# Kernel optimization log

Measured on AMD Instinct MI355X. Metric: run time of the kernel, lower is better.

## Reference

```python
import jax, jax.numpy as jnp
import numpy as np

B, C, H, W = 2, 64, 270, 480
CQ = C // 8


def _distance_weight(n):
    i = jnp.arange(n, dtype=jnp.float32)
    d = i[None, :] - i[:, None]  # j - i
    return jnp.exp(-(d * d) / (2.0 * (n * n / 4.0)))  # [n, n]


def setup_inputs() -> dict:
    key = jax.random.key(0)
    ks = jax.random.split(key, 8)
    s = 0.05
    return {
        "x": jax.random.normal(ks[0], (B, C, H, W), jnp.float32),
        "Wq": jax.random.normal(ks[1], (CQ, C), jnp.float32) * s,
        "bq": jax.random.normal(ks[2], (CQ,), jnp.float32) * s,
        "Wk": jax.random.normal(ks[3], (CQ, C), jnp.float32) * s,
        "bk": jax.random.normal(ks[4], (CQ,), jnp.float32) * s,
        "Wv": jax.random.normal(ks[5], (C, C), jnp.float32) * s,
        "bv": jax.random.normal(ks[6], (C,), jnp.float32) * s,
        "gamma": jax.random.normal(ks[7], (), jnp.float32) * 0.3,
        "dw_h": _distance_weight(H),  # [H, H] non-trainable buffer
        "dw_w": _distance_weight(W),  # [W, W] non-trainable buffer
    }


def reference(x, Wq, bq, Wk, bk, Wv, bv, gamma, dw_h, dw_w):
    # 1x1 convs == per-pixel linear projections
    q = jnp.einsum('oc,bchw->bohw', Wq, x) + bq[None, :, None, None]  # [B,CQ,H,W]
    k = jnp.einsum('oc,bchw->bohw', Wk, x) + bk[None, :, None, None]  # [B,CQ,H,W]
    v = jnp.einsum('oc,bchw->bohw', Wv, x) + bv[None, :, None, None]  # [B,C,H,W]

    height, width = x.shape[2], x.shape[3]
    neg_inf = jnp.float32(-jnp.inf)

    # row (H-direction) energy: queries/keys along the height axis per column w
    e_h = jnp.einsum('bchw,bcgw->bwhg', q, k) * dw_h[None, None]  # [B,W,H,H]
    # diagonal -inf mask (dw_h diag == 1, so order of mul is immaterial)
    eye_h = jnp.eye(height, dtype=bool)
    e_h = jnp.where(eye_h[None, None], neg_inf, e_h)
    e_h = jnp.transpose(e_h, (0, 2, 1, 3))  # [B,H,W,H]

    # column (W-direction) energy along the width axis per row h
    e_w = jnp.einsum('bchw,bchv->bhwv', q, k) * dw_w[None, None]  # [B,H,W,W]

    # joint softmax over concatenated H and W directions
    att = jax.nn.softmax(jnp.concatenate([e_h, e_w], axis=3), axis=3)  # [B,H,W,H+W]
    att_h = jnp.transpose(att[:, :, :, :height], (0, 2, 1, 3))  # [B,W,H,H]
    att_w = att[:, :, :, height:]  # [B,H,W,W]

    out_h = jnp.einsum('bcgw,bwhg->bchw', v, att_h)  # [B,C,H,W]
    out_w = jnp.einsum('bchv,bhwv->bchw', v, att_w)  # [B,C,H,W]

    return gamma * (out_h + out_w) + x
```

## Files before the change

kernel.cpp:

```cpp
#include <hip/hip_runtime.h>
#include <hip/hip_bf16.h>

namespace {

constexpr int B  = 2;
constexpr int C  = 64;
constexpr int CQ = 8;
constexpr int H  = 270;
constexpr int W  = 480;
constexpr int HW = H * W;
constexpr float INVH2 = 2.0f / (270.0f * 270.0f);
constexpr float INVW2 = 2.0f / (480.0f * 480.0f);

typedef __attribute__((ext_vector_type(4))) float f32x4;
typedef __attribute__((ext_vector_type(8))) short short8;
typedef __attribute__((ext_vector_type(4))) unsigned int uint4v;

__device__ __forceinline__ float bits2f(unsigned short u) {
  union { unsigned int i; float f; } cv;
  cv.i = ((unsigned int)u) << 16;
  return cv.f;
}

__device__ __forceinline__ unsigned short f2bf(float f) {
  union { __hip_bfloat16 b; unsigned short u; } cv;
  cv.b = __float2bfloat16(f);
  return cv.u;
}

__device__ __forceinline__ unsigned int pack2(float a, float b) {
  return ((unsigned int)f2bf(b) << 16) | (unsigned int)f2bf(a);
}

__device__ __forceinline__ short8 pack_p(const float p0[4], const float p1[4]) {
  uint4v pw;
  pw[0] = pack2(p0[0], p0[1]);
  pw[1] = pack2(p0[2], p0[3]);
  pw[2] = pack2(p1[0], p1[1]);
  pw[3] = pack2(p1[2], p1[3]);
  return __builtin_bit_cast(short8, pw);
}


__global__ __launch_bounds__(256)
void k_qkv(const float* __restrict__ x,
           const float* __restrict__ Wq, const float* __restrict__ bq,
           const float* __restrict__ Wk, const float* __restrict__ bk,
           const float* __restrict__ Wv, const float* __restrict__ bv,
           unsigned short* __restrict__ qwp, unsigned short* __restrict__ kwp,
           unsigned short* __restrict__ qhp, unsigned short* __restrict__ khp,
           unsigned short* __restrict__ v, unsigned short* __restrict__ vt) {
  __shared__ __align__(16) float wql[CQ * C];
  __shared__ __align__(16) float wkl[CQ * C];
  __shared__ __align__(16) float wvl[C * C];
  __shared__ float bql[CQ], bkl[CQ], bvl[C];
  const int tid = threadIdx.x;
  for (int i = tid; i < CQ * C; i += 256) { wql[i] = Wq[i]; wkl[i] = Wk[i]; }
  for (int i = tid; i < C * C; i += 256) wvl[i] = Wv[i];
  if (tid < CQ) { bql[tid] = bq[tid]; bkl[tid] = bk[tid]; }
  if (tid < C) bvl[tid] = bv[tid];
  __syncthreads();
  const int pix = blockIdx.x * 256 + tid;
  if (pix >= B * HW) return;
  const int b = pix / HW;
  const int r = pix - b * HW;
  const int h = r / W;
  const int w = r - h * W;

  float qa[CQ], ka[CQ], va[C];
#pragma unroll
  for (int o = 0; o < CQ; ++o) { qa[o] = bql[o]; ka[o] = bkl[o]; }
#pragma unroll
  for (int o = 0; o < C; ++o) va[o] = bvl[o];

  const float* xp = x + (size_t)b * C * HW + r;
  for (int c = 0; c < C; c += 4) {
    const float x0 = xp[(size_t)(c + 0) * HW];
    const float x1 = xp[(size_t)(c + 1) * HW];
    const float x2 = xp[(size_t)(c + 2) * HW];
    const float x3 = xp[(size_t)(c + 3) * HW];
#pragma unroll
    for (int o = 0; o < CQ; ++o) {
      const float4 a = *(const float4*)(wql + o * C + c);
      qa[o] = fmaf(a.w, x3, fmaf(a.z, x2, fmaf(a.y, x1, fmaf(a.x, x0, qa[o]))));
      const float4 bb = *(const float4*)(wkl + o * C + c);
      ka[o] = fmaf(bb.w, x3, fmaf(bb.z, x2, fmaf(bb.y, x1, fmaf(bb.x, x0, ka[o]))));
    }
#pragma unroll
    for (int o = 0; o < C; ++o) {
      const float4 cc = *(const float4*)(wvl + o * C + c);
      va[o] = fmaf(cc.w, x3, fmaf(cc.z, x2, fmaf(cc.y, x1, fmaf(cc.x, x0, va[o]))));
    }
  }

  uint4 qp4, kp4;
  qp4.x = pack2(qa[0], qa[1]); qp4.y = pack2(qa[2], qa[3]);
  qp4.z = pack2(qa[4], qa[5]); qp4.w = pack2(qa[6], qa[7]);
  kp4.x = pack2(ka[0], ka[1]); kp4.y = pack2(ka[2], ka[3]);
  kp4.z = pack2(ka[4], ka[5]); kp4.w = pack2(ka[6], ka[7]);
  *(uint4*)(qwp + (size_t)pix * 8) = qp4;
  *(uint4*)(kwp + (size_t)pix * 8) = kp4;
  const size_t tbase = ((size_t)b * W + w) * H + h;
  *(uint4*)(qhp + tbase * 8) = qp4;
  *(uint4*)(khp + tbase * 8) = kp4;

  unsigned short* vp = v + (size_t)b * C * HW + r;
#pragma unroll
  for (int o = 0; o < C; ++o) vp[(size_t)o * HW] = f2bf(va[o]);
  unsigned short* vtp = vt + tbase * C;
#pragma unroll
  for (int j = 0; j < 16; ++j) {
    ushort4 u;
    u.x = f2bf(va[4 * j + 0]);
    u.y = f2bf(va[4 * j + 1]);
    u.z = f2bf(va[4 * j + 2]);
    u.w = f2bf(va[4 * j + 3]);
    *(ushort4*)(vtp + 4 * j) = u;
  }
}

constexpr int VSW = 494;

__global__ __launch_bounds__(512, 1)
void k_outw(const unsigned short* __restrict__ qwp,
            const unsigned short* __restrict__ kwp,
            const unsigned short* __restrict__ v,
            unsigned short* __restrict__ ow, float* __restrict__ Sw) {
  __shared__ __align__(16) unsigned short vbs[64 * VSW];
  __shared__ __align__(16) unsigned short kls[480 * 8];
  const int h = blockIdx.x >> 1, z = blockIdx.x & 1;
  const int b = blockIdx.y;
  const int tid = threadIdx.x;
  const size_t rowbase = ((size_t)b * H + h) * W;

  const unsigned short* vrow = v + (size_t)b * C * HW + (size_t)h * W;
  for (int idx = tid; idx < 64 * 120; idx += 512) {
    const int c = idx / 120, s4 = (idx - c * 120) * 4;
    const int u = s4 & 31;
    const int t = (u < 16) ? ((u >> 2) * 8) : (((u - 16) >> 2) * 8 + 4);
    *(ushort4*)(vbs + c * VSW + (s4 & ~31) + t) =
        *(const ushort4*)(vrow + (size_t)c * HW + s4);
  }
  for (int g = tid; g < 480; g += 512)
    *(uint4*)(kls + g * 8) = *(const uint4*)(kwp + (rowbase + g) * 8);

  const int lane = tid & 63, wv = tid >> 6;
  const int l15 = lane & 15, quad = lane >> 4;
  const int chunk = z * 8 + wv;
  const bool active = chunk < 15;
  const int m0 = chunk * 32;

  short8 qa0 = short8{0, 0, 0, 0, 0, 0, 0, 0};
  short8 qa1 = short8{0, 0, 0, 0, 0, 0, 0, 0};
  if (quad == 0 && active) {
    qa0 = *(const short8*)(qwp + (rowbase + m0 + l15) * 8);
    qa1 = *(const short8*)(qwp + (rowbase + m0 + 16 + l15) * 8);
  }

  f32x4 acc[2][4];
  float Sacc[2] = {0.0f, 0.0f};
#pragma unroll
  for (int mt = 0; mt < 2; ++mt)
#pragma unroll
    for (int ct = 0; ct < 4; ++ct)
#pragma unroll
      for (int rr = 0; rr < 4; ++rr) acc[mt][ct][rr] = 0.0f;

  __syncthreads();

  if (active) {
    for (int ci = 0; ci < 15; ++ci) {
      const int sc = ci * 32;
      short8 kb0 = short8{0, 0, 0, 0, 0, 0, 0, 0};
      short8 kb1 = short8{0, 0, 0, 0, 0, 0, 0, 0};
      if (quad == 0) {
        kb0 = *(const short8*)(kls + (sc + l15) * 8);
        kb1 = *(const short8*)(kls + (sc + 16 + l15) * 8);
      }
      const f32x4 z4 = f32x4{0.f, 0.f, 0.f, 0.f};
      const f32x4 E00 = __builtin_amdgcn_mfma_f32_16x16x32_bf16(kb0, qa0, z4, 0, 0, 0);
      const f32x4 E01 = __builtin_amdgcn_mfma_f32_16x16x32_bf16(kb1, qa0, z4, 0, 0, 0);
      const f32x4 E10 = __builtin_amdgcn_mfma_f32_16x16x32_bf16(kb0, qa1, z4, 0, 0, 0);
      const f32x4 E11 = __builtin_amdgcn_mfma_f32_16x16x32_bf16(kb1, qa1, z4, 0, 0, 0);
      short8 vb[4];
#pragma unroll
      for (int ct = 0; ct < 4; ++ct)
        vb[ct] = *(const short8*)(vbs + (ct * 16 + l15) * VSW + sc + quad * 8);
#pragma unroll
      for (int mt = 0; mt < 2; ++mt) {
        const int m = m0 + mt * 16 + l15;
        const f32x4 Ea = mt ? E10 : E00;
        const f32x4 Eb = mt ? E11 : E01;
        float p0[4], p1[4];
#pragma unroll
        for (int rr = 0; rr < 4; ++rr) {
          const float d0 = (float)(m - (sc + quad * 4 + rr));
          const float d1 = d0 - 16.0f;
          p0[rr] = __expf(Ea[rr] * __expf(-(d0 * d0) * INVW2));
          p1[rr] = __expf(Eb[rr] * __expf(-(d1 * d1) * INVW2));
          Sacc[mt] += p0[rr] + p1[rr];
        }
        const short8 pa = pack_p(p0, p1);
#pragma unroll
        for (int ct = 0; ct < 4; ++ct)
          acc[mt][ct] = __builtin_amdgcn_mfma_f32_16x16x32_bf16(pa, vb[ct], acc[mt][ct], 0, 0, 0);
      }
    }

#pragma unroll
    for (int mt = 0; mt < 2; ++mt) {
      float s = Sacc[mt];
      s += __shfl_xor(s, 16);
      s += __shfl_xor(s, 32);
      if (lane < 16) Sw[rowbase + m0 + mt * 16 + l15] = s;
    }
  }

  __syncthreads();
  unsigned short* ob = vbs;
  if (active) {
#pragma unroll
    for (int mt = 0; mt < 2; ++mt)
#pragma unroll
      for (int ct = 0; ct < 4; ++ct)
#pragma unroll
        for (int rr = 0; rr < 4; ++rr)
          ob[(ct * 16 + l15) * VSW + m0 + mt * 16 + quad * 4 + rr] = f2bf(acc[mt][ct][rr]);
  }
  __syncthreads();
  unsigned short* og = ow + ((size_t)b * H + h) * C * W;
  const int mlo = z ? 256 : 0;
  const int nu = z ? 112 : 128;
  for (int idx = tid; idx < 64 * nu; idx += 512) {
    const int c = idx / nu, i = idx - c * nu;
    *(unsigned int*)(og + (size_t)c * W + mlo + 2 * i) =
        *(const unsigned int*)(ob + c * VSW + mlo + 2 * i);
  }
}

constexpr int VSH = 302;

__global__ __launch_bounds__(320, 1)
void k_outh(const unsigned short* __restrict__ qhp,
            const unsigned short* __restrict__ khp,
            const unsigned short* __restrict__ vt,
            unsigned short* __restrict__ oht, float* __restrict__ Sht) {
  __shared__ __align__(16) unsigned short vbs[64 * VSH];
  __shared__ __align__(16) unsigned short kls[288 * 8];
  const int w = blockIdx.x >> 1, z = blockIdx.x & 1;
  const int b = blockIdx.y;
  const int tid = threadIdx.x;
  const size_t colbase = ((size_t)b * W + w) * H;

  const unsigned short* vtb = vt + colbase * C;
  for (int idx = tid; idx < 288 * 16; idx += 320) {
    const int g = idx >> 4, c4 = (idx & 15) * 4;
    ushort4 vv = make_ushort4(0, 0, 0, 0);
    if (g < H) vv = *(const ushort4*)(vtb + (size_t)g * C + c4);
    const int u = g & 31;
    const int t = (u < 16) ? ((u >> 2) * 8 + (u & 3))
                           : (((u - 16) >> 2) * 8 + 4 + (u & 3));
    const int slot = (g & ~31) + t;
    vbs[(c4 + 0) * VSH + slot] = vv.x;
    vbs[(c4 + 1) * VSH + slot] = vv.y;
    vbs[(c4 + 2) * VSH + slot] = vv.z;
    vbs[(c4 + 3) * VSH + slot] = vv.w;
  }
  for (int g = tid; g < 288; g += 320)
    *(uint4*)(kls + g * 8) =
        *(const uint4*)(khp + (colbase + min(g, H - 1)) * 8);

  const int lane = tid & 63, wv = tid >> 6;
  const int l15 = lane & 15, quad = lane >> 4;
  const int chunk = z * 5 + wv;
  const bool active = chunk < 9;
  const int m0 = chunk * 32;

  short8 qa0 = short8{0, 0, 0, 0, 0, 0, 0, 0};
  short8 qa1 = short8{0, 0, 0, 0, 0, 0, 0, 0};
  if (quad == 0 && active) {
    qa0 = *(const short8*)(qhp + (colbase + min(m0 + l15, H - 1)) * 8);
    qa1 = *(const short8*)(qhp + (colbase + min(m0 + 16 + l15, H - 1)) * 8);
  }

  f32x4 acc[2][4];
  float Sacc[2] = {0.0f, 0.0f};
#pragma unroll
  for (int mt = 0; mt < 2; ++mt)
#pragma unroll
    for (int ct = 0; ct < 4; ++ct)
#pragma unroll
      for (int rr = 0; rr < 4; ++rr) acc[mt][ct][rr] = 0.0f;

  __syncthreads();

  if (active) {
    for (int ci = 0; ci < 9; ++ci) {
      const int gc = ci * 32;
      short8 kb0 = short8{0, 0, 0, 0, 0, 0, 0, 0};
      short8 kb1 = short8{0, 0, 0, 0, 0, 0, 0, 0};
      if (quad == 0) {
        kb0 = *(const short8*)(kls + (gc + l15) * 8);
        kb1 = *(const short8*)(kls + (gc + 16 + l15) * 8);
      }
      const f32x4 z4 = f32x4{0.f, 0.f, 0.f, 0.f};
      const f32x4 E00 = __builtin_amdgcn_mfma_f32_16x16x32_bf16(kb0, qa0, z4, 0, 0, 0);
      const f32x4 E01 = __builtin_amdgcn_mfma_f32_16x16x32_bf16(kb1, qa0, z4, 0, 0, 0);
      const f32x4 E10 = __builtin_amdgcn_mfma_f32_16x16x32_bf16(kb0, qa1, z4, 0, 0, 0);
      const f32x4 E11 = __builtin_amdgcn_mfma_f32_16x16x32_bf16(kb1, qa1, z4, 0, 0, 0);
      short8 vb[4];
#pragma unroll
      for (int ct = 0; ct < 4; ++ct)
        vb[ct] = *(const short8*)(vbs + (ct * 16 + l15) * VSH + gc + quad * 8);
#pragma unroll
      for (int mt = 0; mt < 2; ++mt) {
        const int m = m0 + mt * 16 + l15;
        const f32x4 Ea = mt ? E10 : E00;
        const f32x4 Eb = mt ? E11 : E01;
        float p0[4], p1[4];
#pragma unroll
        for (int rr = 0; rr < 4; ++rr) {
          const int g0 = gc + quad * 4 + rr;
          const int g1 = g0 + 16;
          const float d0 = (float)(m - g0);
          const float d1 = d0 - 16.0f;
          p0[rr] = (g0 < H && g0 != m)
                       ? __expf(Ea[rr] * __expf(-(d0 * d0) * INVH2)) : 0.0f;
          p1[rr] = (g1 < H && g1 != m)
                       ? __expf(Eb[rr] * __expf(-(d1 * d1) * INVH2)) : 0.0f;
          Sacc[mt] += p0[rr] + p1[rr];
        }
        const short8 pa = pack_p(p0, p1);
#pragma unroll
        for (int ct = 0; ct < 4; ++ct)
          acc[mt][ct] = __builtin_amdgcn_mfma_f32_16x16x32_bf16(pa, vb[ct], acc[mt][ct], 0, 0, 0);
      }
    }

#pragma unroll
    for (int mt = 0; mt < 2; ++mt) {
      float s = Sacc[mt];
      s += __shfl_xor(s, 16);
      s += __shfl_xor(s, 32);
      const int m = m0 + mt * 16 + l15;
      if (lane < 16 && m < H) Sht[colbase + m] = s;
    }
  }

  __syncthreads();
  unsigned short* ob = vbs;
  if (active) {
#pragma unroll
    for (int mt = 0; mt < 2; ++mt)
#pragma unroll
      for (int ct = 0; ct < 4; ++ct)
#pragma unroll
        for (int rr = 0; rr < 4; ++rr)
          ob[(ct * 16 + l15) * VSH + m0 + mt * 16 + quad * 4 + rr] = f2bf(acc[mt][ct][rr]);
  }
  __syncthreads();
  unsigned short* og = oht + ((size_t)b * W + w) * C * H;
  const int mlo = z ? 160 : 0;
  const int nu = z ? 55 : 80;
  for (int idx = tid; idx < 64 * nu; idx += 320) {
    const int c = idx / nu, i = idx - c * nu;
    *(unsigned int*)(og + (size_t)c * H + mlo + 2 * i) =
        *(const unsigned int*)(ob + c * VSH + mlo + 2 * i);
  }
}

__global__ __launch_bounds__(256)
void k_combine(const unsigned short* __restrict__ oht,
               const unsigned short* __restrict__ ow,
               const float* __restrict__ Sht, const float* __restrict__ Sw,
               const float* __restrict__ x,
               const float* __restrict__ gp,
               float* __restrict__ out) {
  __shared__ float tile[32][33];
  const int b = blockIdx.z >> 6, c = blockIdx.z & 63;
  const int w0 = blockIdx.x * 32, h0 = blockIdx.y * 32;
  const int tx = threadIdx.x, ty = threadIdx.y;
#pragma unroll
  for (int i = 0; i < 4; ++i) {
    const int wl = ty + i * 8;
    const int hh = h0 + tx;
    float val = 0.0f;
    if (hh < H) val = bits2f(oht[(((size_t)b * W + (w0 + wl)) * C + c) * H + hh]);
    tile[wl][tx] = val;
  }
  __syncthreads();
  const float gamma = *gp;
#pragma unroll
  for (int i = 0; i < 4; ++i) {
    const int hl = ty + i * 8;
    const int hh = h0 + hl;
    if (hh < H) {
      const int ww = w0 + tx;
      const float uh = tile[tx][hl];
      const float uw = bits2f(ow[(((size_t)b * H + hh) * C + c) * W + ww]);
      const size_t si = ((size_t)b * H + hh) * W + ww;
      const float Z = Sht[((size_t)b * W + ww) * H + hh] + Sw[si];
      const float invZ = __builtin_amdgcn_rcpf(Z);
      const size_t xi = ((size_t)b * C + c) * HW + (size_t)hh * W + ww;
      out[xi] = fmaf(gamma * invZ, uh + uw, x[xi]);
    }
  }
}

}

extern "C" void kernel_launch(void* const* d_in, const int* in_sizes, int n_in,
                              void* d_out, int out_size, void* d_ws, size_t ws_size,
                              hipStream_t stream) {
  (void)in_sizes; (void)n_in; (void)out_size; (void)ws_size;
  const float* x  = (const float*)d_in[0];
  const float* Wq = (const float*)d_in[1];
  const float* bq = (const float*)d_in[2];
  const float* Wk = (const float*)d_in[3];
  const float* bk = (const float*)d_in[4];
  const float* Wv = (const float*)d_in[5];
  const float* bv = (const float*)d_in[6];
  const float* gp = (const float*)d_in[7];
  float* out = (float*)d_out;

  char* p = (char*)d_ws;
  auto take = [&](size_t bytes) -> void* {
    char* r = p;
    p += (bytes + 255) & ~(size_t)255;
    return (void*)r;
  };
  unsigned short* qwp = (unsigned short*)take(sizeof(unsigned short) * (size_t)B * HW * 8);
  unsigned short* kwp = (unsigned short*)take(sizeof(unsigned short) * (size_t)B * HW * 8);
  unsigned short* qhp = (unsigned short*)take(sizeof(unsigned short) * (size_t)B * HW * 8);
  unsigned short* khp = (unsigned short*)take(sizeof(unsigned short) * (size_t)B * HW * 8);
  unsigned short* v   = (unsigned short*)take(sizeof(unsigned short) * (size_t)B * C * HW);
  unsigned short* vt  = (unsigned short*)take(sizeof(unsigned short) * (size_t)B * C * HW);
  unsigned short* oht = (unsigned short*)take(sizeof(unsigned short) * (size_t)B * C * HW);
  unsigned short* owb = (unsigned short*)take(sizeof(unsigned short) * (size_t)B * C * HW);
  float* Sht = (float*)take(sizeof(float) * (size_t)B * HW);
  float* Sw  = (float*)take(sizeof(float) * (size_t)B * HW);

  hipLaunchKernelGGL(k_qkv, dim3((B * HW + 255) / 256), dim3(256), 0, stream,
                     x, Wq, bq, Wk, bk, Wv, bv, qwp, kwp, qhp, khp, v, vt);
  hipLaunchKernelGGL(k_outh, dim3(2 * W, B), dim3(320), 0, stream,
                     qhp, khp, vt, oht, Sht);
  hipLaunchKernelGGL(k_outw, dim3(2 * H, B), dim3(512), 0, stream,
                     qwp, kwp, v, owb, Sw);
  hipLaunchKernelGGL(k_combine, dim3(W / 32, (H + 31) / 32, B * C), dim3(32, 8), 0, stream,
                     oht, owb, Sht, Sw, x, gp, out);
}
```

Baseline: 445.8 us.

## Use one 9-wave block per column in k_outh and compute energies per m-tile

k_outh now launches one 576-thread block per (column, batch) instead of two 320-thread half-blocks. All nine waves are active, so the V/K staging into shared memory happens once per column instead of twice, and the idle wave is gone. In both attention kernels, the four energy MFMAs are moved inside the m-tile loop, presumably to lower register pressure by keeping only two energy tiles live at a time. The tradeoff is larger blocks at one block per CU, which may reduce scheduling flexibility and occupancy.

```diff
diff --git a/kernel.cpp b/kernel.cpp
--- a/kernel.cpp
+++ b/kernel.cpp
@@ -177,20 +177,17 @@
         kb0 = *(const short8*)(kls + (sc + l15) * 8);
         kb1 = *(const short8*)(kls + (sc + 16 + l15) * 8);
       }
-      const f32x4 z4 = f32x4{0.f, 0.f, 0.f, 0.f};
-      const f32x4 E00 = __builtin_amdgcn_mfma_f32_16x16x32_bf16(kb0, qa0, z4, 0, 0, 0);
-      const f32x4 E01 = __builtin_amdgcn_mfma_f32_16x16x32_bf16(kb1, qa0, z4, 0, 0, 0);
-      const f32x4 E10 = __builtin_amdgcn_mfma_f32_16x16x32_bf16(kb0, qa1, z4, 0, 0, 0);
-      const f32x4 E11 = __builtin_amdgcn_mfma_f32_16x16x32_bf16(kb1, qa1, z4, 0, 0, 0);
       short8 vb[4];
 #pragma unroll
       for (int ct = 0; ct < 4; ++ct)
         vb[ct] = *(const short8*)(vbs + (ct * 16 + l15) * VSW + sc + quad * 8);
+      const f32x4 z4 = f32x4{0.f, 0.f, 0.f, 0.f};
 #pragma unroll
       for (int mt = 0; mt < 2; ++mt) {
+        const short8 qa = mt ? qa1 : qa0;
+        const f32x4 Ea = __builtin_amdgcn_mfma_f32_16x16x32_bf16(kb0, qa, z4, 0, 0, 0);
+        const f32x4 Eb = __builtin_amdgcn_mfma_f32_16x16x32_bf16(kb1, qa, z4, 0, 0, 0);
         const int m = m0 + mt * 16 + l15;
-        const f32x4 Ea = mt ? E10 : E00;
-        const f32x4 Eb = mt ? E11 : E01;
         float p0[4], p1[4];
 #pragma unroll
         for (int rr = 0; rr < 4; ++rr) {
@@ -240,20 +237,20 @@
 
 constexpr int VSH = 302;
 
-__global__ __launch_bounds__(320, 1)
+__global__ __launch_bounds__(576, 1)
 void k_outh(const unsigned short* __restrict__ qhp,
             const unsigned short* __restrict__ khp,
             const unsigned short* __restrict__ vt,
             unsigned short* __restrict__ oht, float* __restrict__ Sht) {
   __shared__ __align__(16) unsigned short vbs[64 * VSH];
   __shared__ __align__(16) unsigned short kls[288 * 8];
-  const int w = blockIdx.x >> 1, z = blockIdx.x & 1;
+  const int w = blockIdx.x;
   const int b = blockIdx.y;
   const int tid = threadIdx.x;
   const size_t colbase = ((size_t)b * W + w) * H;
 
   const unsigned short* vtb = vt + colbase * C;
-  for (int idx = tid; idx < 288 * 16; idx += 320) {
+  for (int idx = tid; idx < 288 * 16; idx += 576) {
     const int g = idx >> 4, c4 = (idx & 15) * 4;
     ushort4 vv = make_ushort4(0, 0, 0, 0);
     if (g < H) vv = *(const ushort4*)(vtb + (size_t)g * C + c4);
@@ -266,19 +263,17 @@
     vbs[(c4 + 2) * VSH + slot] = vv.z;
     vbs[(c4 + 3) * VSH + slot] = vv.w;
   }
-  for (int g = tid; g < 288; g += 320)
+  for (int g = tid; g < 288; g += 576)
     *(uint4*)(kls + g * 8) =
         *(const uint4*)(khp + (colbase + min(g, H - 1)) * 8);
 
   const int lane = tid & 63, wv = tid >> 6;
   const int l15 = lane & 15, quad = lane >> 4;
-  const int chunk = z * 5 + wv;
-  const bool active = chunk < 9;
-  const int m0 = chunk * 32;
+  const int m0 = wv * 32;
 
   short8 qa0 = short8{0, 0, 0, 0, 0, 0, 0, 0};
   short8 qa1 = short8{0, 0, 0, 0, 0, 0, 0, 0};
-  if (quad == 0 && active) {
+  if (quad == 0) {
     qa0 = *(const short8*)(qhp + (colbase + min(m0 + l15, H - 1)) * 8);
     qa1 = *(const short8*)(qhp + (colbase + min(m0 + 16 + l15, H - 1)) * 8);
   }
@@ -294,78 +289,69 @@
 
   __syncthreads();
 
-  if (active) {
-    for (int ci = 0; ci < 9; ++ci) {
-      const int gc = ci * 32;
-      short8 kb0 = short8{0, 0, 0, 0, 0, 0, 0, 0};
-      short8 kb1 = short8{0, 0, 0, 0, 0, 0, 0, 0};
-      if (quad == 0) {
-        kb0 = *(const short8*)(kls + (gc + l15) * 8);
-        kb1 = *(const short8*)(kls + (gc + 16 + l15) * 8);
+  for (int ci = 0; ci < 9; ++ci) {
+    const int gc = ci * 32;
+    short8 kb0 = short8{0, 0, 0, 0, 0, 0, 0, 0};
+    short8 kb1 = short8{0, 0, 0, 0, 0, 0, 0, 0};
+    if (quad == 0) {
+      kb0 = *(const short8*)(kls + (gc + l15) * 8);
+      kb1 = *(const short8*)(kls + (gc + 16 + l15) * 8);
+    }
+    short8 vb[4];
+#pragma unroll
+    for (int ct = 0; ct < 4; ++ct)
+      vb[ct] = *(const short8*)(vbs + (ct * 16 + l15) * VSH + gc + quad * 8);
+    const f32x4 z4 = f32x4{0.f, 0.f, 0.f, 0.f};
+#pragma unroll
+    for (int mt = 0; mt < 2; ++mt) {
+      const short8 qa = mt ? qa1 : qa0;
+      const f32x4 Ea = __builtin_amdgcn_mfma_f32_16x16x32_bf16(kb0, qa, z4, 0, 0, 0);
+      const f32x4 Eb = __builtin_amdgcn_mfma_f32_16x16x32_bf16(kb1, qa, z4, 0, 0, 0);
+      const int m = m0 + mt * 16 + l15;
+      float p0[4], p1[4];
+#pragma unroll
+      for (int rr = 0; rr < 4; ++rr) {
+        const int g0 = gc + quad * 4 + rr;
+        const int g1 = g0 + 16;
+        const float d0 = (float)(m - g0);
+        const float d1 = d0 - 16.0f;
+        p0[rr] = (g0 < H && g0 != m)
+                     ? __expf(Ea[rr] * __expf(-(d0 * d0) * INVH2)) : 0.0f;
+        p1[rr] = (g1 < H && g1 != m)
+                     ? __expf(Eb[rr] * __expf(-(d1 * d1) * INVH2)) : 0.0f;
+        Sacc[mt] += p0[rr] + p1[rr];
       }
-      const f32x4 z4 = f32x4{0.f, 0.f, 0.f, 0.f};
-      const f32x4 E00 = __builtin_amdgcn_mfma_f32_16x16x32_bf16(kb0, qa0, z4, 0, 0, 0);
-      const f32x4 E01 = __builtin_amdgcn_mfma_f32_16x16x32_bf16(kb1, qa0, z4, 0, 0, 0);
-      const f32x4 E10 = __builtin_amdgcn_mfma_f32_16x16x32_bf16(kb0, qa1, z4, 0, 0, 0);
-      const f32x4 E11 = __builtin_amdgcn_mfma_f32_16x16x32_bf16(kb1, qa1, z4, 0, 0, 0);
-      short8 vb[4];
+      const short8 pa = pack_p(p0, p1);
 #pragma unroll
       for (int ct = 0; ct < 4; ++ct)
-        vb[ct] = *(const short8*)(vbs + (ct * 16 + l15) * VSH + gc + quad * 8);
-#pragma unroll
-      for (int mt = 0; mt < 2; ++mt) {
-        const int m = m0 + mt * 16 + l15;
-        const f32x4 Ea = mt ? E10 : E00;
-        const f32x4 Eb = mt ? E11 : E01;
-        float p0[4], p1[4];
-#pragma unroll
-        for (int rr = 0; rr < 4; ++rr) {
-          const int g0 = gc + quad * 4 + rr;
-          const int g1 = g0 + 16;
-          const float d0 = (float)(m - g0);
-          const float d1 = d0 - 16.0f;
-          p0[rr] = (g0 < H && g0 != m)
-                       ? __expf(Ea[rr] * __expf(-(d0 * d0) * INVH2)) : 0.0f;
-          p1[rr] = (g1 < H && g1 != m)
-                       ? __expf(Eb[rr] * __expf(-(d1 * d1) * INVH2)) : 0.0f;
-          Sacc[mt] += p0[rr] + p1[rr];
-        }
-        const short8 pa = pack_p(p0, p1);
-#pragma unroll
-        for (int ct = 0; ct < 4; ++ct)
-          acc[mt][ct] = __builtin_amdgcn_mfma_f32_16x16x32_bf16(pa, vb[ct], acc[mt][ct], 0, 0, 0);
-      }
-    }
-
-#pragma unroll
-    for (int mt = 0; mt < 2; ++mt) {
-      float s = Sacc[mt];
-      s += __shfl_xor(s, 16);
-      s += __shfl_xor(s, 32);
-      const int m = m0 + mt * 16 + l15;
-      if (lane < 16 && m < H) Sht[colbase + m] = s;
-    }
+        acc[mt][ct] = __builtin_amdgcn_mfma_f32_16x16x32_bf16(pa, vb[ct], acc[mt][ct], 0, 0, 0);
+    }
+  }
+
+#pragma unroll
+  for (int mt = 0; mt < 2; ++mt) {
+    float s = Sacc[mt];
+    s += __shfl_xor(s, 16);
+    s += __shfl_xor(s, 32);
+    const int m = m0 + mt * 16 + l15;
+    if (lane < 16 && m < H) Sht[colbase + m] = s;
   }
 
   __syncthreads();
   unsigned short* ob = vbs;
-  if (active) {
-#pragma unroll
-    for (int mt = 0; mt < 2; ++mt)
-#pragma unroll
-      for (int ct = 0; ct < 4; ++ct)
-#pragma unroll
-        for (int rr = 0; rr < 4; ++rr)
-          ob[(ct * 16 + l15) * VSH + m0 + mt * 16 + quad * 4 + rr] = f2bf(acc[mt][ct][rr]);
-  }
+#pragma unroll
+  for (int mt = 0; mt < 2; ++mt)
+#pragma unroll
+    for (int ct = 0; ct < 4; ++ct)
+#pragma unroll
+      for (int rr = 0; rr < 4; ++rr)
+        ob[(ct * 16 + l15) * VSH + m0 + mt * 16 + quad * 4 + rr] = f2bf(acc[mt][ct][rr]);
   __syncthreads();
   unsigned short* og = oht + ((size_t)b * W + w) * C * H;
-  const int mlo = z ? 160 : 0;
-  const int nu = z ? 55 : 80;
-  for (int idx = tid; idx < 64 * nu; idx += 320) {
-    const int c = idx / nu, i = idx - c * nu;
-    *(unsigned int*)(og + (size_t)c * H + mlo + 2 * i) =
-        *(const unsigned int*)(ob + c * VSH + mlo + 2 * i);
+  for (int idx = tid; idx < 64 * 135; idx += 576) {
+    const int c = idx / 135, hp = idx - c * 135;
+    *(unsigned int*)(og + (size_t)c * H + 2 * hp) =
+        *(const unsigned int*)(ob + c * VSH + 2 * hp);
   }
 }
 
@@ -442,7 +428,7 @@
 
   hipLaunchKernelGGL(k_qkv, dim3((B * HW + 255) / 256), dim3(256), 0, stream,
                      x, Wq, bq, Wk, bk, Wv, bv, qwp, kwp, qhp, khp, v, vt);
-  hipLaunchKernelGGL(k_outh, dim3(2 * W, B), dim3(320), 0, stream,
+  hipLaunchKernelGGL(k_outh, dim3(W, B), dim3(576), 0, stream,
                      qhp, khp, vt, oht, Sht);
   hipLaunchKernelGGL(k_outw, dim3(2 * H, B), dim3(512), 0, stream,
                      qwp, kwp, v, owb, Sw);
```

New measurement: 444.4 us. Within noise of the previous version (-0.3%).
